# Performance work log

Measured on AMD Instinct MI355X. Metric: run time of the kernel, lower is better.

The kernel has to match this reference:

```python
import jax, jax.numpy as jnp
import numpy as np


def _masked_var(x, mask):
    # unbiased variance (torch.var default, ddof=1) over entries where mask==1
    cnt = jnp.sum(mask)
    mean = jnp.sum(x * mask) / jnp.maximum(cnt, 1.0)
    return jnp.sum(mask * (x - mean) ** 2) / jnp.maximum(cnt - 1.0, 1.0)


def setup_inputs() -> dict:
    key = jax.random.key(0)
    ks = jax.random.split(key, 9)
    B, N, F = 4, 8192, 64
    points = jax.random.normal(ks[0], (B, N, 3), dtype=jnp.float32)
    features = jax.random.normal(ks[1], (B, N, F), dtype=jnp.float32)
    leaf_mask = jax.random.randint(ks[2], (B, N), 0, 2).astype(bool)
    W1 = jax.random.normal(ks[3], (64, F + 3), dtype=jnp.float32) * 0.05
    b1 = jax.random.normal(ks[4], (64,), dtype=jnp.float32) * 0.05
    W2 = jax.random.normal(ks[5], (32, 64), dtype=jnp.float32) * 0.05
    b2 = jax.random.normal(ks[6], (32,), dtype=jnp.float32) * 0.05
    W3 = jax.random.normal(ks[7], (1, 32), dtype=jnp.float32) * 0.05
    b3 = jax.random.normal(ks[8], (1,), dtype=jnp.float32) * 0.05
    return {"points": points, "features": features, "leaf_mask": leaf_mask,
            "W1": W1, "b1": b1, "W2": W2, "b2": b2, "W3": W3, "b3": b3}


def reference(points, features, leaf_mask, W1, b1, W2, b2, W3, b3):
    # NOTE: in the original Torch code combined_feat = [feat(F), xyz(3), var(1)]
    # (length F+4) is truncated to expected_input_dim = F+3, so the kNN feature
    # variance is provably dropped. The MLP input is exactly [feat, xyz].
    B, N, _ = points.shape

    def mlp(x):  # x: [N, F+3]
        h = jax.nn.relu(x @ W1.T + b1)
        h = jax.nn.relu(h @ W2.T + b2)
        return jax.nn.sigmoid(h @ W3.T + b3)[:, 0]

    def per_batch(pts, feats, mask):
        maskf = mask.astype(pts.dtype)
        x = jnp.concatenate([feats, pts], axis=-1)  # [N, F+3]
        scores = mlp(x) * maskf  # non-leaf points stay 0
        n_leaf = jnp.sum(maskf)
        scores = jnp.where(n_leaf < 10.0, jnp.zeros_like(scores), scores)

        # separation confidence
        clarity = _masked_var(scores, maskf)
        sel = scores > 0.7
        cnt = jnp.sum(sel.astype(jnp.int32))
        idx = jnp.arange(N)
        order = jnp.argsort(jnp.where(sel, idx, N + idx))  # selected first, in order
        g = pts[order]  # [N,3]
        d = jnp.linalg.norm(g[1:] - g[:-1], axis=1)  # consecutive boundary-point dists
        pair_mask = (jnp.arange(N - 1) < cnt - 1).astype(pts.dtype)
        dvar = _masked_var(d, pair_mask)
        cont = jnp.clip(1.0 / (dvar + 1e-8), 0.0, 1.0)
        cont = jnp.where(cnt > 5, cont, 0.0)
        conf = jnp.clip(clarity * cont, 0.0, 1.0)
        conf = jnp.where(n_leaf == 0.0, 0.0, conf)
        return scores, conf

    boundary_prob, separation_confidence = jax.vmap(per_batch)(points, features, leaf_mask)
    return boundary_prob, features, separation_confidence
```

## Files before the change

### kernel.cpp

```cpp
#include <hip/hip_runtime.h>
#include <hip/hip_bf16.h>
#include <math.h>

#define NB 4
#define NPTS 8192
#define TOTAL_PTS (NB * NPTS)
#define OUT_FEAT_OFF 32768
#define OUT_CONF_OFF (32768 + 2097152)

__device__ __forceinline__ float blockReduceSum256(float v) {
    __shared__ float sred[4];
#pragma unroll
    for (int o = 32; o > 0; o >>= 1) v += __shfl_down(v, o, 64);
    const int w = threadIdx.x >> 6, l = threadIdx.x & 63;
    __syncthreads();
    if (l == 0) sred[w] = v;
    __syncthreads();
    return sred[0] + sred[1] + sred[2] + sred[3];
}

__global__ __launch_bounds__(256) void fused_kernel(
    const float* __restrict__ pts,
    const float* __restrict__ feats,
    const int* __restrict__ mask,
    const float* __restrict__ W1,
    const float* __restrict__ b1,
    const float* __restrict__ W2,
    const float* __restrict__ b2,
    const float* __restrict__ W3,
    const float* __restrict__ b3,
    float* __restrict__ out,
    int* __restrict__ counters,
    float* __restrict__ wsf)
{
    __shared__ float sW1[67 * 64];
    __shared__ float sW2[64 * 32];
    __shared__ float sB1[64];
    __shared__ float sB2[32];
    __shared__ float sW3[32];
    __shared__ float sB3;
    __shared__ int sflag;
    __shared__ int cnts[256];

    const int t = threadIdx.x;

    for (int idx = t; idx < 67 * 64; idx += 256) {
        const int k = idx >> 6, j = idx & 63;
        sW1[idx] = W1[j * 67 + k];
    }
    for (int idx = t; idx < 64 * 32; idx += 256) {
        const int k = idx >> 5, j = idx & 31;
        sW2[idx] = W2[j * 64 + k];
    }
    if (t < 64) sB1[t] = b1[t];
    else if (t < 96) sB2[t - 64] = b2[t - 64];
    else if (t < 128) sW3[t - 96] = W3[t - 96];
    if (t == 0) sB3 = b3[0];

    {
        const float4* fsrc = (const float4*)feats + (size_t)blockIdx.x * 1024;
        float4* fdst = (float4*)(out + OUT_FEAT_OFF) + (size_t)blockIdx.x * 1024;
#pragma unroll
        for (int i = 0; i < 4; ++i)
            fdst[i * 256 + t] = fsrc[i * 256 + t];
    }
    __syncthreads();

    const int wv = t >> 6;
    const int ln = t & 63;
    const int q = ln >> 4;
    const int pi = wv * 16 + (ln & 15);
    const int p = blockIdx.x * 64 + pi;
    const int joff = q * 16;

    float h1[16];
#pragma unroll
    for (int j = 0; j < 16; ++j) h1[j] = sB1[joff + j];

    const float4* fx = (const float4*)feats + (size_t)p * 16;
    for (int kc = 0; kc < 16; ++kc) {
        const float4 xv = fx[kc];
        const float* r0 = &sW1[(4 * kc + 0) * 64 + joff];
        const float* r1 = &sW1[(4 * kc + 1) * 64 + joff];
        const float* r2 = &sW1[(4 * kc + 2) * 64 + joff];
        const float* r3 = &sW1[(4 * kc + 3) * 64 + joff];
#pragma unroll
        for (int j4 = 0; j4 < 4; ++j4) {
            const float4 a = *(const float4*)&r0[4 * j4];
            const float4 b = *(const float4*)&r1[4 * j4];
            const float4 c = *(const float4*)&r2[4 * j4];
            const float4 d = *(const float4*)&r3[4 * j4];
            h1[4*j4+0] = fmaf(xv.x,a.x, fmaf(xv.y,b.x, fmaf(xv.z,c.x, fmaf(xv.w,d.x, h1[4*j4+0]))));
            h1[4*j4+1] = fmaf(xv.x,a.y, fmaf(xv.y,b.y, fmaf(xv.z,c.y, fmaf(xv.w,d.y, h1[4*j4+1]))));
            h1[4*j4+2] = fmaf(xv.x,a.z, fmaf(xv.y,b.z, fmaf(xv.z,c.z, fmaf(xv.w,d.z, h1[4*j4+2]))));
            h1[4*j4+3] = fmaf(xv.x,a.w, fmaf(xv.y,b.w, fmaf(xv.z,c.w, fmaf(xv.w,d.w, h1[4*j4+3]))));
        }
    }
    const float px = pts[(size_t)p * 3 + 0];
    const float py = pts[(size_t)p * 3 + 1];
    const float pz = pts[(size_t)p * 3 + 2];
    {
        const float* r0 = &sW1[64 * 64 + joff];
        const float* r1 = &sW1[65 * 64 + joff];
        const float* r2 = &sW1[66 * 64 + joff];
#pragma unroll
        for (int j4 = 0; j4 < 4; ++j4) {
            const float4 a = *(const float4*)&r0[4 * j4];
            const float4 b = *(const float4*)&r1[4 * j4];
            const float4 c = *(const float4*)&r2[4 * j4];
            h1[4*j4+0] = fmaxf(fmaf(px,a.x, fmaf(py,b.x, fmaf(pz,c.x, h1[4*j4+0]))), 0.f);
            h1[4*j4+1] = fmaxf(fmaf(px,a.y, fmaf(py,b.y, fmaf(pz,c.y, h1[4*j4+1]))), 0.f);
            h1[4*j4+2] = fmaxf(fmaf(px,a.z, fmaf(py,b.z, fmaf(pz,c.z, h1[4*j4+2]))), 0.f);
            h1[4*j4+3] = fmaxf(fmaf(px,a.w, fmaf(py,b.w, fmaf(pz,c.w, h1[4*j4+3]))), 0.f);
        }
    }

    float h2[32];
#pragma unroll
    for (int j = 0; j < 32; ++j) h2[j] = (q == 0) ? sB2[j] : 0.0f;
#pragma unroll
    for (int k = 0; k < 16; ++k) {
        const float hv = h1[k];
        const float* wr = &sW2[(joff + k) * 32];
#pragma unroll
        for (int j4 = 0; j4 < 8; ++j4) {
            const float4 w = *(const float4*)&wr[4 * j4];
            h2[4*j4+0] = fmaf(hv, w.x, h2[4*j4+0]);
            h2[4*j4+1] = fmaf(hv, w.y, h2[4*j4+1]);
            h2[4*j4+2] = fmaf(hv, w.z, h2[4*j4+2]);
            h2[4*j4+3] = fmaf(hv, w.w, h2[4*j4+3]);
        }
    }
#pragma unroll
    for (int j = 0; j < 32; ++j) h2[j] += __shfl_xor(h2[j], 16, 64);
#pragma unroll
    for (int j = 0; j < 32; ++j) h2[j] += __shfl_xor(h2[j], 32, 64);

    float z = sB3;
#pragma unroll
    for (int j4 = 0; j4 < 8; ++j4) {
        const float4 w = *(const float4*)&sW3[4 * j4];
        z = fmaf(fmaxf(h2[4*j4+0], 0.f), w.x, z);
        z = fmaf(fmaxf(h2[4*j4+1], 0.f), w.y, z);
        z = fmaf(fmaxf(h2[4*j4+2], 0.f), w.z, z);
        z = fmaf(fmaxf(h2[4*j4+3], 0.f), w.w, z);
    }
    float sc = 1.0f / (1.0f + expf(-z));
    if (mask[p] == 0) sc = 0.0f;
    if (q == 0) out[p] = sc;

    const int batch = blockIdx.x >> 7;
    __syncthreads();
    if (t == 0) {
        const int old = __hip_atomic_fetch_add(&counters[batch], 1,
                                               __ATOMIC_ACQ_REL,
                                               __HIP_MEMORY_SCOPE_AGENT);
        sflag = (old == 127);
    }
    __syncthreads();
    if (!sflag) return;
    __builtin_amdgcn_fence(__ATOMIC_ACQUIRE, "agent");

    float* scores = out + (size_t)batch * NPTS;
    const float* P = pts + (size_t)batch * NPTS * 3;
    const int* M = mask + (size_t)batch * NPTS;
    float* g = wsf + (size_t)batch * 40960;
    float* dd = g + 3 * NPTS;

    float s[32];
    unsigned int mbits = 0;
#pragma unroll
    for (int i = 0; i < 8; ++i) {
        const float4 s4 = ((const float4*)scores)[t * 8 + i];
        s[4*i+0] = s4.x; s[4*i+1] = s4.y; s[4*i+2] = s4.z; s[4*i+3] = s4.w;
        const int4 m4 = ((const int4*)M)[t * 8 + i];
        mbits |= (m4.x != 0 ? 1u : 0u) << (4*i+0);
        mbits |= (m4.y != 0 ? 1u : 0u) << (4*i+1);
        mbits |= (m4.z != 0 ? 1u : 0u) << (4*i+2);
        mbits |= (m4.w != 0 ? 1u : 0u) << (4*i+3);
    }

    float ss = 0.f;
#pragma unroll
    for (int i = 0; i < 32; ++i) ss += s[i];
    const float nleaf = blockReduceSum256((float)__popc(mbits));
    const float ssum = blockReduceSum256(ss);

    if (nleaf < 10.0f) {
        const float4 z4 = {0.f, 0.f, 0.f, 0.f};
#pragma unroll
        for (int i = 0; i < 8; ++i) ((float4*)scores)[t * 8 + i] = z4;
        if (t == 0) out[OUT_CONF_OFF + batch] = 0.0f;
        return;
    }

    const float mean = ssum / fmaxf(nleaf, 1.0f);
    float vs = 0.f;
#pragma unroll
    for (int i = 0; i < 32; ++i) {
        if (mbits & (1u << i)) {
            const float d0 = s[i] - mean;
            vs += d0 * d0;
        }
    }
    const float clarity = blockReduceSum256(vs) / fmaxf(nleaf - 1.0f, 1.0f);

    int c0 = 0;
#pragma unroll
    for (int i = 0; i < 32; ++i) c0 += (s[i] > 0.7f);
    cnts[t] = c0;
    __syncthreads();
    for (int off = 1; off < 256; off <<= 1) {
        const int v = cnts[t];
        const int a = (t >= off) ? cnts[t - off] : 0;
        __syncthreads();
        cnts[t] = v + a;
        __syncthreads();
    }
    const int cnt = cnts[255];
    int pos = cnts[t] - c0;
#pragma unroll
    for (int i = 0; i < 32; ++i) {
        if (s[i] > 0.7f) {
            const int idx = t * 32 + i;
            g[3 * pos + 0] = P[3 * idx + 0];
            g[3 * pos + 1] = P[3 * idx + 1];
            g[3 * pos + 2] = P[3 * idx + 2];
            ++pos;
        }
    }
    __syncthreads();

    const int npair = cnt - 1;
    float dsum = 0.f;
    for (int i = t; i < npair; i += 256) {
        const float ax = g[3 * i + 0] - g[3 * i + 3];
        const float ay = g[3 * i + 1] - g[3 * i + 4];
        const float az = g[3 * i + 2] - g[3 * i + 5];
        const float d0 = sqrtf(ax * ax + ay * ay + az * az);
        dd[i] = d0;
        dsum += d0;
    }
    const float dtot = blockReduceSum256(dsum);
    const float npf = (float)npair;
    const float dmean = dtot / fmaxf(npf, 1.0f);
    float dv = 0.f;
    for (int i = t; i < npair; i += 256) {
        const float e = dd[i] - dmean;
        dv += e * e;
    }
    const float dvar = blockReduceSum256(dv) / fmaxf(npf - 1.0f, 1.0f);

    float cont = fminf(fmaxf(1.0f / (dvar + 1e-8f), 0.0f), 1.0f);
    if (!(cnt > 5)) cont = 0.0f;
    const float conf = fminf(fmaxf(clarity * cont, 0.0f), 1.0f);
    if (t == 0) out[OUT_CONF_OFF + batch] = conf;
}

extern "C" void kernel_launch(void* const* d_in, const int* in_sizes, int n_in,
                              void* d_out, int out_size, void* d_ws, size_t ws_size,
                              hipStream_t stream) {
    const float* points   = (const float*)d_in[0];
    const float* features = (const float*)d_in[1];
    const int*   leafmask = (const int*)d_in[2];
    const float* W1 = (const float*)d_in[3];
    const float* b1 = (const float*)d_in[4];
    const float* W2 = (const float*)d_in[5];
    const float* b2 = (const float*)d_in[6];
    const float* W3 = (const float*)d_in[7];
    const float* b3 = (const float*)d_in[8];
    float* out = (float*)d_out;
    int* counters = (int*)d_ws;
    float* wsf = (float*)d_ws + 64;

    (void)hipMemsetAsync(d_ws, 0, 64, stream);
    fused_kernel<<<512, 256, 0, stream>>>(
        points, features, leafmask, W1, b1, W2, b2, W3, b3, out, counters, wsf);
}
```

Before: 107.4 us.

## Read MLP weights as wave-uniform scalar loads instead of staging in LDS

Each wave now owns a 16-wide slice of the hidden layer for all 64 points. Because the slice index is made wave-uniform with readfirstlane, the W1/W2 reads can become scalar (SMEM) loads from global memory, so the per-block transposed weight copy into shared memory is removed. Features are staged through LDS once, while the global-to-output copy is in flight, and partial layer-2 sums are reduced across waves through shared memory rather than with shuffles. In exchange it adds an extra barrier, leaves three waves idle during the final layer, and raises register pressure from holding 16 float4 inputs per thread.

```diff
diff --git a/kernel.cpp b/kernel.cpp
--- a/kernel.cpp
+++ b/kernel.cpp
@@ -1,10 +1,8 @@
 #include <hip/hip_runtime.h>
-#include <hip/hip_bf16.h>
 #include <math.h>
 
 #define NB 4
 #define NPTS 8192
-#define TOTAL_PTS (NB * NPTS)
 #define OUT_FEAT_OFF 32768
 #define OUT_CONF_OFF (32768 + 2097152)
 
@@ -33,121 +31,98 @@
     int* __restrict__ counters,
     float* __restrict__ wsf)
 {
-    __shared__ float sW1[67 * 64];
-    __shared__ float sW2[64 * 32];
-    __shared__ float sB1[64];
-    __shared__ float sB2[32];
-    __shared__ float sW3[32];
-    __shared__ float sB3;
+    __shared__ float sX[64 * 68];
+    __shared__ float sH[3 * 64 * 36];
     __shared__ int sflag;
     __shared__ int cnts[256];
 
     const int t = threadIdx.x;
-
-    for (int idx = t; idx < 67 * 64; idx += 256) {
-        const int k = idx >> 6, j = idx & 63;
-        sW1[idx] = W1[j * 67 + k];
-    }
-    for (int idx = t; idx < 64 * 32; idx += 256) {
-        const int k = idx >> 5, j = idx & 31;
-        sW2[idx] = W2[j * 64 + k];
-    }
-    if (t < 64) sB1[t] = b1[t];
-    else if (t < 96) sB2[t - 64] = b2[t - 64];
-    else if (t < 128) sW3[t - 96] = W3[t - 96];
-    if (t == 0) sB3 = b3[0];
+    const int ln = t & 63;
+    const int q = __builtin_amdgcn_readfirstlane(t >> 6);
 
     {
         const float4* fsrc = (const float4*)feats + (size_t)blockIdx.x * 1024;
         float4* fdst = (float4*)(out + OUT_FEAT_OFF) + (size_t)blockIdx.x * 1024;
 #pragma unroll
-        for (int i = 0; i < 4; ++i)
-            fdst[i * 256 + t] = fsrc[i * 256 + t];
-    }
-    __syncthreads();
-
-    const int wv = t >> 6;
-    const int ln = t & 63;
-    const int q = ln >> 4;
-    const int pi = wv * 16 + (ln & 15);
-    const int p = blockIdx.x * 64 + pi;
-    const int joff = q * 16;
-
-    float h1[16];
-#pragma unroll
-    for (int j = 0; j < 16; ++j) h1[j] = sB1[joff + j];
-
-    const float4* fx = (const float4*)feats + (size_t)p * 16;
-    for (int kc = 0; kc < 16; ++kc) {
-        const float4 xv = fx[kc];
-        const float* r0 = &sW1[(4 * kc + 0) * 64 + joff];
-        const float* r1 = &sW1[(4 * kc + 1) * 64 + joff];
-        const float* r2 = &sW1[(4 * kc + 2) * 64 + joff];
-        const float* r3 = &sW1[(4 * kc + 3) * 64 + joff];
-#pragma unroll
-        for (int j4 = 0; j4 < 4; ++j4) {
-            const float4 a = *(const float4*)&r0[4 * j4];
-            const float4 b = *(const float4*)&r1[4 * j4];
-            const float4 c = *(const float4*)&r2[4 * j4];
-            const float4 d = *(const float4*)&r3[4 * j4];
-            h1[4*j4+0] = fmaf(xv.x,a.x, fmaf(xv.y,b.x, fmaf(xv.z,c.x, fmaf(xv.w,d.x, h1[4*j4+0]))));
-            h1[4*j4+1] = fmaf(xv.x,a.y, fmaf(xv.y,b.y, fmaf(xv.z,c.y, fmaf(xv.w,d.y, h1[4*j4+1]))));
-            h1[4*j4+2] = fmaf(xv.x,a.z, fmaf(xv.y,b.z, fmaf(xv.z,c.z, fmaf(xv.w,d.z, h1[4*j4+2]))));
-            h1[4*j4+3] = fmaf(xv.x,a.w, fmaf(xv.y,b.w, fmaf(xv.z,c.w, fmaf(xv.w,d.w, h1[4*j4+3]))));
-        }
-    }
+        for (int i = 0; i < 4; ++i) {
+            const int e = i * 256 + t;
+            const float4 v = fsrc[e];
+            fdst[e] = v;
+            *(float4*)&sX[(e >> 4) * 68 + (e & 15) * 4] = v;
+        }
+    }
+    __syncthreads();
+
+    const int p = blockIdx.x * 64 + ln;
+
+    float4 xv[16];
+#pragma unroll
+    for (int kc = 0; kc < 16; ++kc)
+        xv[kc] = *(const float4*)&sX[ln * 68 + kc * 4];
     const float px = pts[(size_t)p * 3 + 0];
     const float py = pts[(size_t)p * 3 + 1];
     const float pz = pts[(size_t)p * 3 + 2];
-    {
-        const float* r0 = &sW1[64 * 64 + joff];
-        const float* r1 = &sW1[65 * 64 + joff];
-        const float* r2 = &sW1[66 * 64 + joff];
-#pragma unroll
-        for (int j4 = 0; j4 < 4; ++j4) {
-            const float4 a = *(const float4*)&r0[4 * j4];
-            const float4 b = *(const float4*)&r1[4 * j4];
-            const float4 c = *(const float4*)&r2[4 * j4];
-            h1[4*j4+0] = fmaxf(fmaf(px,a.x, fmaf(py,b.x, fmaf(pz,c.x, h1[4*j4+0]))), 0.f);
-            h1[4*j4+1] = fmaxf(fmaf(px,a.y, fmaf(py,b.y, fmaf(pz,c.y, h1[4*j4+1]))), 0.f);
-            h1[4*j4+2] = fmaxf(fmaf(px,a.z, fmaf(py,b.z, fmaf(pz,c.z, h1[4*j4+2]))), 0.f);
-            h1[4*j4+3] = fmaxf(fmaf(px,a.w, fmaf(py,b.w, fmaf(pz,c.w, h1[4*j4+3]))), 0.f);
-        }
-    }
-
-    float h2[32];
-#pragma unroll
-    for (int j = 0; j < 32; ++j) h2[j] = (q == 0) ? sB2[j] : 0.0f;
-#pragma unroll
-    for (int k = 0; k < 16; ++k) {
-        const float hv = h1[k];
-        const float* wr = &sW2[(joff + k) * 32];
-#pragma unroll
-        for (int j4 = 0; j4 < 8; ++j4) {
-            const float4 w = *(const float4*)&wr[4 * j4];
-            h2[4*j4+0] = fmaf(hv, w.x, h2[4*j4+0]);
-            h2[4*j4+1] = fmaf(hv, w.y, h2[4*j4+1]);
-            h2[4*j4+2] = fmaf(hv, w.z, h2[4*j4+2]);
-            h2[4*j4+3] = fmaf(hv, w.w, h2[4*j4+3]);
-        }
-    }
-#pragma unroll
-    for (int j = 0; j < 32; ++j) h2[j] += __shfl_xor(h2[j], 16, 64);
-#pragma unroll
-    for (int j = 0; j < 32; ++j) h2[j] += __shfl_xor(h2[j], 32, 64);
-
-    float z = sB3;
-#pragma unroll
-    for (int j4 = 0; j4 < 8; ++j4) {
-        const float4 w = *(const float4*)&sW3[4 * j4];
-        z = fmaf(fmaxf(h2[4*j4+0], 0.f), w.x, z);
-        z = fmaf(fmaxf(h2[4*j4+1], 0.f), w.y, z);
-        z = fmaf(fmaxf(h2[4*j4+2], 0.f), w.z, z);
-        z = fmaf(fmaxf(h2[4*j4+3], 0.f), w.w, z);
-    }
-    float sc = 1.0f / (1.0f + expf(-z));
-    if (mask[p] == 0) sc = 0.0f;
-    if (q == 0) out[p] = sc;
+
+    const int jq = q * 16;
+    float h1[16];
+#pragma unroll
+    for (int jj = 0; jj < 16; ++jj) {
+        const float* wr = W1 + (size_t)(jq + jj) * 67;
+        float a = b1[jq + jj];
+#pragma unroll
+        for (int kc = 0; kc < 16; ++kc) {
+            a = fmaf(xv[kc].x, wr[4 * kc + 0], a);
+            a = fmaf(xv[kc].y, wr[4 * kc + 1], a);
+            a = fmaf(xv[kc].z, wr[4 * kc + 2], a);
+            a = fmaf(xv[kc].w, wr[4 * kc + 3], a);
+        }
+        a = fmaf(px, wr[64], a);
+        a = fmaf(py, wr[65], a);
+        a = fmaf(pz, wr[66], a);
+        h1[jj] = fmaxf(a, 0.f);
+    }
+
+    float p2[32];
+#pragma unroll
+    for (int j = 0; j < 32; ++j) {
+        const float* wr = W2 + (size_t)j * 64 + jq;
+        float a = 0.f;
+#pragma unroll
+        for (int kk = 0; kk < 16; ++kk) a = fmaf(h1[kk], wr[kk], a);
+        p2[j] = a;
+    }
+
+    if (q != 0) {
+        float* dst = &sH[(size_t)((q - 1) * 64 + ln) * 36];
+#pragma unroll
+        for (int m = 0; m < 8; ++m) {
+            float4 v;
+            v.x = p2[4 * m + 0]; v.y = p2[4 * m + 1];
+            v.z = p2[4 * m + 2]; v.w = p2[4 * m + 3];
+            *(float4*)&dst[4 * m] = v;
+        }
+    }
+    __syncthreads();
+
+    if (q == 0) {
+#pragma unroll
+        for (int qq = 0; qq < 3; ++qq) {
+            const float* src = &sH[(size_t)(qq * 64 + ln) * 36];
+#pragma unroll
+            for (int m = 0; m < 8; ++m) {
+                const float4 v = *(const float4*)&src[4 * m];
+                p2[4 * m + 0] += v.x; p2[4 * m + 1] += v.y;
+                p2[4 * m + 2] += v.z; p2[4 * m + 3] += v.w;
+            }
+        }
+        float z = b3[0];
+#pragma unroll
+        for (int j = 0; j < 32; ++j)
+            z = fmaf(fmaxf(p2[j] + b2[j], 0.f), W3[j], z);
+        float sc = 1.0f / (1.0f + expf(-z));
+        if (mask[p] == 0) sc = 0.0f;
+        out[p] = sc;
+    }
 
     const int batch = blockIdx.x >> 7;
     __syncthreads();
```

Result: slower. 117.0 us (+8.9%).
